# Kernel optimization log

Measured on AMD Instinct MI355X. Metric: run time of the kernel, lower is better.

The kernel has to match this reference:

```python
import jax, jax.numpy as jnp
import numpy as np

EPS = 1e-06
ALPHA = 0.1
BETA = 0.1
B, N = 2048, 4096


def setup_inputs() -> dict:
    key = jax.random.key(0)
    k1, k2, k3, k4 = jax.random.split(key, 4)
    yhat = jax.random.normal(k1, (B, N), dtype=jnp.float32)
    y = jax.random.uniform(k2, (B, N), dtype=jnp.float32)
    batch_mask = jax.random.bernoulli(k3, 0.5, (B, N))
    # neighbor matrix: entries in {0, 1, 2} remapped to {0, alpha, beta}
    raw = jax.random.randint(k4, (N, N), 0, 3)
    spots_neighbors = jnp.where(raw == 1, ALPHA, jnp.where(raw == 2, BETA, 0.0)).astype(jnp.float32)
    return {"yhat": yhat, "y": y, "batch_mask": batch_mask, "spots_neighbors": spots_neighbors}


def reference(yhat, y, batch_mask, spots_neighbors):
    # squared error everywhere: [B, N]
    sq = jnp.square(y - yhat)
    # spatial_loss[:, i] = sq @ spots_neighbors[i]  ==  sq @ spots_neighbors.T
    spatial = jnp.einsum('bn,in->bi', sq, spots_neighbors)
    # masked_error at masked positions equals sq there, so total = sq + spatial, masked
    total = sq + spatial
    m = batch_mask.astype(sq.dtype)
    cnt = jnp.sum(m)
    loss = jnp.sqrt(jnp.sum(total * m) / cnt + EPS)
    return loss
```

## Files before the change

kernel.cpp:

```cpp
#include <hip/hip_runtime.h>
#include <hip/hip_bf16.h>

typedef int   i32x4  __attribute__((ext_vector_type(4)));
typedef int   i32x8  __attribute__((ext_vector_type(8)));
typedef float f32x16 __attribute__((ext_vector_type(16)));

#define BB 2048
#define NN 4096
#define NT 32

#define SQT_OFF ((size_t)0)
#define MT_OFF  ((size_t)16*1024*1024)
#define SCAL_OFF ((size_t)32*1024*1024)
#define PART_OFF (SCAL_OFF + 1024)
#define PART2_OFF (PART_OFF + 16384)
#define NBLK_P1 (64*32)
#define NBLK_G  256

__device__ __forceinline__ unsigned f32_to_e4m3(float f) {
  if (f >= 448.0f) return 0x7eu;
  if (f < 0.015625f) return (unsigned)(int)rintf(f * 512.0f);
  unsigned u = __float_as_uint(f);
  unsigned r = u + 0x7ffffu + ((u >> 20) & 1u);
  int e = (int)((r >> 23) & 0xff) - 127;
  return ((unsigned)(e + 7) << 3) | ((r >> 20) & 7u);
}

struct P1Acc { float s1, cnt; };

template<int MODE>
__device__ __forceinline__ P1Acc p1_load_phase(
    const float* __restrict__ yhat, const float* __restrict__ y,
    const void* __restrict__ maskraw, unsigned short (*tile)[66],
    int b0, int n0, int brw, int nq)
{
  float4 yv[4], hv[4];
  float mv[4][4];
  #pragma unroll
  for (int rr = 0; rr < 4; ++rr) {
    int brow = brw + rr * 16;
    size_t idx = (size_t)(b0 + brow) * NN + n0 + nq;
    yv[rr] = *(const float4*)(y + idx);
    hv[rr] = *(const float4*)(yhat + idx);
    if (MODE == 0) {
      uchar4 t = *(const uchar4*)((const unsigned char*)maskraw + idx);
      mv[rr][0] = (float)t.x; mv[rr][1] = (float)t.y;
      mv[rr][2] = (float)t.z; mv[rr][3] = (float)t.w;
    } else if (MODE == 1) {
      int4 t = *(const int4*)((const int*)maskraw + idx);
      mv[rr][0] = (t.x != 0) ? 1.f : 0.f; mv[rr][1] = (t.y != 0) ? 1.f : 0.f;
      mv[rr][2] = (t.z != 0) ? 1.f : 0.f; mv[rr][3] = (t.w != 0) ? 1.f : 0.f;
    } else {
      float4 t = *(const float4*)((const float*)maskraw + idx);
      mv[rr][0] = (t.x != 0.f) ? 1.f : 0.f; mv[rr][1] = (t.y != 0.f) ? 1.f : 0.f;
      mv[rr][2] = (t.z != 0.f) ? 1.f : 0.f; mv[rr][3] = (t.w != 0.f) ? 1.f : 0.f;
    }
  }
  float s1 = 0.f, cnt = 0.f;
  #pragma unroll
  for (int rr = 0; rr < 4; ++rr) {
    int brow = brw + rr * 16;
    float d0 = yv[rr].x - hv[rr].x, d1 = yv[rr].y - hv[rr].y;
    float d2 = yv[rr].z - hv[rr].z, d3 = yv[rr].w - hv[rr].w;
    float sq[4] = { d0*d0, d1*d1, d2*d2, d3*d3 };
    unsigned t0 = f32_to_e4m3(sq[0]) | (mv[rr][0] != 0.f ? 0x3800u : 0u);
    unsigned t1 = f32_to_e4m3(sq[1]) | (mv[rr][1] != 0.f ? 0x3800u : 0u);
    unsigned t2 = f32_to_e4m3(sq[2]) | (mv[rr][2] != 0.f ? 0x3800u : 0u);
    unsigned t3 = f32_to_e4m3(sq[3]) | (mv[rr][3] != 0.f ? 0x3800u : 0u);
    *(uint2*)(&tile[brow][nq]) = make_uint2(t0 | (t1 << 16), t2 | (t3 << 16));
    s1 += sq[0]*mv[rr][0] + sq[1]*mv[rr][1] + sq[2]*mv[rr][2] + sq[3]*mv[rr][3];
    cnt += mv[rr][0] + mv[rr][1] + mv[rr][2] + mv[rr][3];
  }
  return { s1, cnt };
}

__global__ __launch_bounds__(256, 2) void k_pass1(
    const float* __restrict__ yhat, const float* __restrict__ y,
    const void* __restrict__ maskraw,
    unsigned char* __restrict__ SQT, unsigned char* __restrict__ MT,
    float2* __restrict__ part)
{
  __shared__ unsigned short tile[64][66];
  __shared__ float red[8];
  __shared__ unsigned mflag;
  const int tid = threadIdx.x;
  const int lane = tid & 63;
  if (tid == 0) mflag = 0;
  __syncthreads();
  {
    uint4 mb = *(const uint4*)((const unsigned char*)maskraw + tid * 16);
    unsigned f = 0;
    unsigned ws[4] = { mb.x, mb.y, mb.z, mb.w };
    #pragma unroll
    for (int q = 0; q < 4; ++q) {
      unsigned w = ws[q];
      bool h3f = ((w & 0xffu) == 0x3fu) | (((w >> 8) & 0xffu) == 0x3fu) |
                 (((w >> 16) & 0xffu) == 0x3fu) | ((w >> 24) == 0x3fu);
      f |= h3f ? 1u : 0u;
      f |= ((w & 0xffffff00u) != 0u) ? 2u : 0u;
    }
    bool a1 = __any((int)(f & 1)), a2 = __any((int)(f & 2));
    if (lane == 0) {
      unsigned g = (a1 ? 1u : 0u) | (a2 ? 2u : 0u);
      if (g) atomicOr(&mflag, g);
    }
  }
  __syncthreads();
  const unsigned mf = mflag;
  const int mode = (mf & 1) ? 2 : ((mf & 2) ? 0 : 1);

  const int n0 = blockIdx.x * 64;
  const int b0 = blockIdx.y * 64;
  const int nq = (tid & 15) * 4;
  const int brw = tid >> 4;
  P1Acc a;
  if (mode == 0)      a = p1_load_phase<0>(yhat, y, maskraw, tile, b0, n0, brw, nq);
  else if (mode == 1) a = p1_load_phase<1>(yhat, y, maskraw, tile, b0, n0, brw, nq);
  else                a = p1_load_phase<2>(yhat, y, maskraw, tile, b0, n0, brw, nq);
  __syncthreads();
  {
    int nrow = tid >> 2;
    int cb   = tid & 3;
    int grow = n0 + nrow;
    unsigned us[4], um[4];
    #pragma unroll
    for (int q = 0; q < 4; ++q) {
      unsigned v0 = tile[cb*16 + q*4 + 0][nrow];
      unsigned v1 = tile[cb*16 + q*4 + 1][nrow];
      unsigned v2 = tile[cb*16 + q*4 + 2][nrow];
      unsigned v3 = tile[cb*16 + q*4 + 3][nrow];
      us[q] = (v0 & 0xffu) | ((v1 & 0xffu) << 8) | ((v2 & 0xffu) << 16) | ((v3 & 0xffu) << 24);
      um[q] = (v0 >> 8) | ((v1 >> 8) << 8) | ((v2 >> 8) << 16) | ((v3 >> 8) << 24);
    }
    size_t off = (size_t)(grow >> 7) * 262144 + (size_t)(b0 >> 6) * 8192
               + (size_t)cb * 2048 + (size_t)(grow & 127) * 16;
    *(uint4*)(SQT + off) = make_uint4(us[0], us[1], us[2], us[3]);
    *(uint4*)(MT  + off) = make_uint4(um[0], um[1], um[2], um[3]);
  }
  float s1 = a.s1, cnt = a.cnt;
  #pragma unroll
  for (int off = 32; off >= 1; off >>= 1) {
    s1  += __shfl_down(s1,  off, 64);
    cnt += __shfl_down(cnt, off, 64);
  }
  int wv = tid >> 6;
  if ((tid & 63) == 0) { red[wv] = s1; red[4 + wv] = cnt; }
  __syncthreads();
  if (tid == 0)
    part[blockIdx.y * gridDim.x + blockIdx.x] =
        make_float2(red[0] + red[1] + red[2] + red[3],
                    red[4] + red[5] + red[6] + red[7]);
}

__global__ __launch_bounds__(512, 2) void k_gemm(
    const unsigned char* __restrict__ MT,
    const unsigned char* __restrict__ SQT,
    const float* __restrict__ W,
    float* __restrict__ part2)
{
  extern __shared__ char lds[];
  const int tid = threadIdx.x;
  const int lane = tid & 63;
  const int wave = tid >> 6;
  const int wm  = wave >> 2;
  const int wmB = wm * 128;
  const int wnB = (wave & 3) * 64;
  const int l31 = lane & 31;
  const int lch2 = (lane >> 5) * 2;

  const int bid = blockIdx.x;
  const int swz = (bid & 7) * 32 + (bid >> 3);
  const int nb = swz & 15, ib = swz >> 4;
  const int n0 = nb * 256, i0 = ib * 256;

  const unsigned char* aSrc = MT  + (size_t)ib * 524288;
  const unsigned char* bSrc = SQT + (size_t)nb * 524288;
  const int tid16 = tid * 16;

#define STG(c, s) \
  _Pragma("unroll") for (int j = 0; j < 2; ++j) { \
    __builtin_amdgcn_global_load_lds( \
      (const __attribute__((address_space(1))) unsigned int*)( \
          aSrc + (size_t)j * 262144 + (size_t)(s) * 8192 + tid16), \
      (__attribute__((address_space(3))) unsigned int*)(lds + (c) * 16384 + j * 8192 + tid16), \
      16, 0, 0); \
    __builtin_amdgcn_global_load_lds( \
      (const __attribute__((address_space(1))) unsigned int*)( \
          bSrc + (size_t)j * 262144 + (size_t)(s) * 8192 + tid16), \
      (__attribute__((address_space(3))) unsigned int*)(lds + 65536 + (c) * 16384 + j * 8192 + tid16), \
      16, 0, 0); }

#define WPF(k) { \
    float4 wtmp = *((const float4*)(W + (size_t)(i0 + (k)*8 + (tid >> 6)) * NN + n0) + (tid & 63)); \
    asm volatile("" :: "v"(wtmp.x), "v"(wtmp.y), "v"(wtmp.z), "v"(wtmp.w)); }

#define RDA2(d0, d1, bufA, mgb) { \
    const char* p0 = (bufA) + wm*8192 + lch2*2048 + ((mgb)*32 + l31)*16; \
    const char* p1 = p0 + 512; \
    i32x4 lo0 = *(const i32x4*)p0; i32x4 hi0 = *(const i32x4*)(p0 + 2048); \
    i32x4 lo1 = *(const i32x4*)p1; i32x4 hi1 = *(const i32x4*)(p1 + 2048); \
    d0 = __builtin_shufflevector(lo0, hi0, 0, 1, 2, 3, 4, 5, 6, 7); \
    d1 = __builtin_shufflevector(lo1, hi1, 0, 1, 2, 3, 4, 5, 6, 7); }
#define RDB(d, bufB, ng) { \
    int rg = wnB + (ng)*32; \
    const char* p = (bufB) + (rg >> 7)*8192 + lch2*2048 + ((rg & 127) + l31)*16; \
    i32x4 lo = *(const i32x4*)p; i32x4 hi = *(const i32x4*)(p + 2048); \
    d = __builtin_shufflevector(lo, hi, 0, 1, 2, 3, 4, 5, 6, 7); }

#define MM(mg, ng, A, B) \
  acc[mg][ng] = __builtin_amdgcn_mfma_scale_f32_32x32x64_f8f6f4( \
      A, B, acc[mg][ng], 0, 0, 0, 0x7f7f7f7f, 0, 0x7f7f7f7f)

#define TILE_BODY(c) { \
    const char* bufA = lds + (c) * 16384; \
    const char* bufB = lds + 65536 + (c) * 16384; \
    i32x8 a0, a1, a2, a3, b0, b1; \
    RDA2(a0, a1, bufA, 0); RDB(b0, bufB, 0); \
    RDA2(a2, a3, bufA, 2); RDB(b1, bufB, 1); \
    MM(0, 0, a0, b0); MM(1, 0, a1, b0); MM(2, 0, a2, b0); MM(3, 0, a3, b0); \
    MM(0, 1, a0, b1); MM(1, 1, a1, b1); MM(2, 1, a2, b1); MM(3, 1, a3, b1); }

  f32x16 acc[4][2] = {};

  STG(0, 0); WPF(0);
  STG(1, 1); WPF(1);
  STG(2, 2); WPF(2);

  #pragma unroll 1
  for (int t = 0; t < NT - 2; ++t) {
    asm volatile("s_waitcnt vmcnt(11)" ::: "memory");
    __builtin_amdgcn_s_barrier();
    __builtin_amdgcn_sched_barrier(0);
    if (t < NT - 3) { STG((t + 3) & 3, t + 3); WPF(t + 3); }
    TILE_BODY(t & 3);
  }
  asm volatile("s_waitcnt vmcnt(6)" ::: "memory");
  __builtin_amdgcn_s_barrier();
  __builtin_amdgcn_sched_barrier(0);
  TILE_BODY(2);
  asm volatile("s_waitcnt vmcnt(1)" ::: "memory");
  __builtin_amdgcn_s_barrier();
  __builtin_amdgcn_sched_barrier(0);
  TILE_BODY(3);
#undef STG
#undef WPF
#undef RDA2
#undef RDB
#undef MM
#undef TILE_BODY

  float local = 0.0f;
  #pragma unroll
  for (int mg = 0; mg < 4; ++mg) {
    int rbase = i0 + wmB + mg * 32 + (lane >> 5) * 4;
    #pragma unroll
    for (int ng = 0; ng < 2; ++ng) {
      int nn = n0 + wnB + ng * 32 + l31;
      const float* wp = W + (size_t)rbase * NN + nn;
      #pragma unroll
      for (int reg = 0; reg < 16; ++reg) {
        int roff = (reg & 3) + 8 * (reg >> 2);
        local += acc[mg][ng][reg] * wp[(size_t)roff * NN];
      }
    }
  }
  #pragma unroll
  for (int off = 32; off >= 1; off >>= 1)
    local += __shfl_down(local, off, 64);
  float* wpart = (float*)lds;
  __syncthreads();
  if (lane == 0) wpart[wave] = local;
  __syncthreads();
  if (tid == 0) {
    float s = 0.f;
    #pragma unroll
    for (int i = 0; i < 8; ++i) s += wpart[i];
    part2[bid] = s;
  }
}

__global__ __launch_bounds__(256) void k_finalize(
    const float2* __restrict__ part, const float* __restrict__ part2,
    float* __restrict__ out)
{
  __shared__ float rs[4], rc[4];
  float s1 = 0.f, cnt = 0.f;
  for (int i = threadIdx.x; i < NBLK_P1; i += 256) {
    float2 p = part[i];
    s1 += p.x; cnt += p.y;
  }
  for (int i = threadIdx.x; i < NBLK_G; i += 256)
    s1 += part2[i];
  #pragma unroll
  for (int off = 32; off >= 1; off >>= 1) {
    s1  += __shfl_down(s1,  off, 64);
    cnt += __shfl_down(cnt, off, 64);
  }
  int wv = threadIdx.x >> 6;
  if ((threadIdx.x & 63) == 0) { rs[wv] = s1; rc[wv] = cnt; }
  __syncthreads();
  if (threadIdx.x == 0) {
    float S = rs[0] + rs[1] + rs[2] + rs[3];
    float C = rc[0] + rc[1] + rc[2] + rc[3];
    out[0] = sqrtf(S / C + 1e-6f);
  }
}

__global__ void k_sentinel(float* out) { out[0] = 1.2345e8f; }

extern "C" void kernel_launch(void* const* d_in, const int* in_sizes, int n_in,
                              void* d_out, int out_size, void* d_ws, size_t ws_size,
                              hipStream_t stream) {
  const float* yhat = (const float*)d_in[0];
  const float* y    = (const float*)d_in[1];
  const void*  mask = d_in[2];
  const float* W    = (const float*)d_in[3];
  float* out = (float*)d_out;

  const size_t need = PART2_OFF + (size_t)NBLK_G * 4;
  if (ws_size < need) { k_sentinel<<<1, 1, 0, stream>>>(out); return; }

  char* ws = (char*)d_ws;
  unsigned char* SQT = (unsigned char*)(ws + SQT_OFF);
  unsigned char* MTp = (unsigned char*)(ws + MT_OFF);
  float2* part = (float2*)(ws + PART_OFF);
  float* part2 = (float*)(ws + PART2_OFF);

  (void)hipFuncSetAttribute((const void*)k_gemm,
                            hipFuncAttributeMaxDynamicSharedMemorySize, 131072);

  k_pass1<<<dim3(NN/64, BB/64), 256, 0, stream>>>(yhat, y, mask, SQT, MTp, part);
  k_gemm<<<NBLK_G, 512, 131072, stream>>>(MTp, SQT, W, part2);
  k_finalize<<<1, 256, 0, stream>>>(part, part2, out);
}
```

Before: 72.60 us.

## Load A fragments directly to registers, double-buffer only B in LDS

The GEMM kernel now reads the A operand (mask tile) straight from global memory into per-wave registers instead of staging it through LDS, and keeps only B in a two-stage LDS double buffer, cutting shared memory from 128KB to 32KB. The W prefetch into cache is dropped, the pipeline depth goes from four stages to two with full vmcnt(0) waits each step, and MFMA blocks are wrapped in s_setprio. This reduces LDS traffic and footprint but exposes more global-load latency because the prefetch distance is shorter.

```diff
diff --git a/kernel.cpp b/kernel.cpp
--- a/kernel.cpp
+++ b/kernel.cpp
@@ -173,81 +173,73 @@
   const int nb = swz & 15, ib = swz >> 4;
   const int n0 = nb * 256, i0 = ib * 256;
 
-  const unsigned char* aSrc = MT  + (size_t)ib * 524288;
   const unsigned char* bSrc = SQT + (size_t)nb * 524288;
+  const unsigned char* aLane = MT + (size_t)ib * 524288 + (size_t)wm * 262144
+                             + (size_t)lch2 * 2048 + (size_t)l31 * 16;
   const int tid16 = tid * 16;
 
-#define STG(c, s) \
+#define STG_B(c, s) \
   _Pragma("unroll") for (int j = 0; j < 2; ++j) { \
     __builtin_amdgcn_global_load_lds( \
       (const __attribute__((address_space(1))) unsigned int*)( \
-          aSrc + (size_t)j * 262144 + (size_t)(s) * 8192 + tid16), \
+          bSrc + (size_t)j * 262144 + (size_t)(s) * 8192 + tid16), \
       (__attribute__((address_space(3))) unsigned int*)(lds + (c) * 16384 + j * 8192 + tid16), \
-      16, 0, 0); \
-    __builtin_amdgcn_global_load_lds( \
-      (const __attribute__((address_space(1))) unsigned int*)( \
-          bSrc + (size_t)j * 262144 + (size_t)(s) * 8192 + tid16), \
-      (__attribute__((address_space(3))) unsigned int*)(lds + 65536 + (c) * 16384 + j * 8192 + tid16), \
       16, 0, 0); }
 
-#define WPF(k) { \
-    float4 wtmp = *((const float4*)(W + (size_t)(i0 + (k)*8 + (tid >> 6)) * NN + n0) + (tid & 63)); \
-    asm volatile("" :: "v"(wtmp.x), "v"(wtmp.y), "v"(wtmp.z), "v"(wtmp.w)); }
-
-#define RDA2(d0, d1, bufA, mgb) { \
-    const char* p0 = (bufA) + wm*8192 + lch2*2048 + ((mgb)*32 + l31)*16; \
-    const char* p1 = p0 + 512; \
+#define ALD(dst, s) \
+  _Pragma("unroll") for (int mg = 0; mg < 4; ++mg) { \
+    const unsigned char* p = aLane + (size_t)(s) * 8192 + mg * 512; \
+    i32x4 lo = *(const i32x4*)p; \
+    i32x4 hi = *(const i32x4*)(p + 2048); \
+    dst[mg] = __builtin_shufflevector(lo, hi, 0, 1, 2, 3, 4, 5, 6, 7); }
+
+#define RDB(d0r, d1r, c) { \
+    int rg0 = wnB; \
+    const char* p0 = lds + (c)*16384 + (rg0 >> 7)*8192 + lch2*2048 + ((rg0 & 127) + l31)*16; \
     i32x4 lo0 = *(const i32x4*)p0; i32x4 hi0 = *(const i32x4*)(p0 + 2048); \
+    d0r = __builtin_shufflevector(lo0, hi0, 0, 1, 2, 3, 4, 5, 6, 7); \
+    int rg1 = wnB + 32; \
+    const char* p1 = lds + (c)*16384 + (rg1 >> 7)*8192 + lch2*2048 + ((rg1 & 127) + l31)*16; \
     i32x4 lo1 = *(const i32x4*)p1; i32x4 hi1 = *(const i32x4*)(p1 + 2048); \
-    d0 = __builtin_shufflevector(lo0, hi0, 0, 1, 2, 3, 4, 5, 6, 7); \
-    d1 = __builtin_shufflevector(lo1, hi1, 0, 1, 2, 3, 4, 5, 6, 7); }
-#define RDB(d, bufB, ng) { \
-    int rg = wnB + (ng)*32; \
-    const char* p = (bufB) + (rg >> 7)*8192 + lch2*2048 + ((rg & 127) + l31)*16; \
-    i32x4 lo = *(const i32x4*)p; i32x4 hi = *(const i32x4*)(p + 2048); \
-    d = __builtin_shufflevector(lo, hi, 0, 1, 2, 3, 4, 5, 6, 7); }
-
-#define MM(mg, ng, A, B) \
-  acc[mg][ng] = __builtin_amdgcn_mfma_scale_f32_32x32x64_f8f6f4( \
-      A, B, acc[mg][ng], 0, 0, 0, 0x7f7f7f7f, 0, 0x7f7f7f7f)
-
-#define TILE_BODY(c) { \
-    const char* bufA = lds + (c) * 16384; \
-    const char* bufB = lds + 65536 + (c) * 16384; \
-    i32x8 a0, a1, a2, a3, b0, b1; \
-    RDA2(a0, a1, bufA, 0); RDB(b0, bufB, 0); \
-    RDA2(a2, a3, bufA, 2); RDB(b1, bufB, 1); \
-    MM(0, 0, a0, b0); MM(1, 0, a1, b0); MM(2, 0, a2, b0); MM(3, 0, a3, b0); \
-    MM(0, 1, a0, b1); MM(1, 1, a1, b1); MM(2, 1, a2, b1); MM(3, 1, a3, b1); }
-
+    d1r = __builtin_shufflevector(lo1, hi1, 0, 1, 2, 3, 4, 5, 6, 7); }
+
+#define MFMA8(AF, B0, B1) \
+  __builtin_amdgcn_s_setprio(1); \
+  _Pragma("unroll") for (int mg = 0; mg < 4; ++mg) { \
+    acc[mg][0] = __builtin_amdgcn_mfma_scale_f32_32x32x64_f8f6f4( \
+        AF[mg], B0, acc[mg][0], 0, 0, 0, 0x7f7f7f7f, 0, 0x7f7f7f7f); \
+    acc[mg][1] = __builtin_amdgcn_mfma_scale_f32_32x32x64_f8f6f4( \
+        AF[mg], B1, acc[mg][1], 0, 0, 0, 0x7f7f7f7f, 0, 0x7f7f7f7f); } \
+  __builtin_amdgcn_s_setprio(0)
+
+#define TOPSYNC \
+  asm volatile("s_waitcnt vmcnt(0)" ::: "memory"); \
+  __builtin_amdgcn_s_barrier(); \
+  __builtin_amdgcn_sched_barrier(0)
+
+  i32x8 aX[4], aY[4], b0r, b1r;
   f32x16 acc[4][2] = {};
 
-  STG(0, 0); WPF(0);
-  STG(1, 1); WPF(1);
-  STG(2, 2); WPF(2);
+  ALD(aX, 0);
+  STG_B(0, 0);
 
   #pragma unroll 1
-  for (int t = 0; t < NT - 2; ++t) {
-    asm volatile("s_waitcnt vmcnt(11)" ::: "memory");
-    __builtin_amdgcn_s_barrier();
-    __builtin_amdgcn_sched_barrier(0);
-    if (t < NT - 3) { STG((t + 3) & 3, t + 3); WPF(t + 3); }
-    TILE_BODY(t & 3);
-  }
-  asm volatile("s_waitcnt vmcnt(6)" ::: "memory");
-  __builtin_amdgcn_s_barrier();
-  __builtin_amdgcn_sched_barrier(0);
-  TILE_BODY(2);
-  asm volatile("s_waitcnt vmcnt(1)" ::: "memory");
-  __builtin_amdgcn_s_barrier();
-  __builtin_amdgcn_sched_barrier(0);
-  TILE_BODY(3);
-#undef STG
-#undef WPF
-#undef RDA2
+  for (int tp = 0; tp < NT; tp += 2) {
+    TOPSYNC;
+    ALD(aY, tp + 1);
+    STG_B(1, tp + 1);
+    RDB(b0r, b1r, 0);
+    MFMA8(aX, b0r, b1r);
+    TOPSYNC;
+    if (tp + 2 < NT) { ALD(aX, tp + 2); STG_B(0, tp + 2); }
+    RDB(b0r, b1r, 1);
+    MFMA8(aY, b0r, b1r);
+  }
+#undef STG_B
+#undef ALD
 #undef RDB
-#undef MM
-#undef TILE_BODY
+#undef MFMA8
+#undef TOPSYNC
 
   float local = 0.0f;
   #pragma unroll
@@ -327,9 +319,9 @@
   float* part2 = (float*)(ws + PART2_OFF);
 
   (void)hipFuncSetAttribute((const void*)k_gemm,
-                            hipFuncAttributeMaxDynamicSharedMemorySize, 131072);
+                            hipFuncAttributeMaxDynamicSharedMemorySize, 32768);
 
   k_pass1<<<dim3(NN/64, BB/64), 256, 0, stream>>>(yhat, y, mask, SQT, MTp, part);
-  k_gemm<<<NBLK_G, 512, 131072, stream>>>(MTp, SQT, W, part2);
+  k_gemm<<<NBLK_G, 512, 32768, stream>>>(MTp, SQT, W, part2);
   k_finalize<<<1, 256, 0, stream>>>(part, part2, out);
 }
```

Result: slower. 75.82 us (+4.4%).

## Use 1024-thread GEMM blocks with 2x2 MFMA tiles per wave and 3-stage buffering

Applied to the files above, without the earlier changes.

Doubles the GEMM block to 16 waves so each wave owns a 64x64 output tile (4 accumulators) instead of 128x64 (8). The LDS pipeline drops from 4 stages to 3, and the W prefetch into cache is removed. MFMA sections are wrapped in s_setprio. The aim is more waves to hide latency and lower register pressure, at the cost of each wave doing more LDS reads per MFMA and having shallower prefetch.

```diff
diff --git a/kernel.cpp b/kernel.cpp
--- a/kernel.cpp
+++ b/kernel.cpp
@@ -152,7 +152,7 @@
                     red[4] + red[5] + red[6] + red[7]);
 }
 
-__global__ __launch_bounds__(512, 2) void k_gemm(
+__global__ __launch_bounds__(1024) void k_gemm(
     const unsigned char* __restrict__ MT,
     const unsigned char* __restrict__ SQT,
     const float* __restrict__ W,
@@ -163,8 +163,7 @@
   const int lane = tid & 63;
   const int wave = tid >> 6;
   const int wm  = wave >> 2;
-  const int wmB = wm * 128;
-  const int wnB = (wave & 3) * 64;
+  const int wn  = wave & 3;
   const int l31 = lane & 31;
   const int lch2 = (lane >> 5) * 2;
 
@@ -176,92 +175,72 @@
   const unsigned char* aSrc = MT  + (size_t)ib * 524288;
   const unsigned char* bSrc = SQT + (size_t)nb * 524288;
   const int tid16 = tid * 16;
-
-#define STG(c, s) \
-  _Pragma("unroll") for (int j = 0; j < 2; ++j) { \
-    __builtin_amdgcn_global_load_lds( \
-      (const __attribute__((address_space(1))) unsigned int*)( \
-          aSrc + (size_t)j * 262144 + (size_t)(s) * 8192 + tid16), \
-      (__attribute__((address_space(3))) unsigned int*)(lds + (c) * 16384 + j * 8192 + tid16), \
-      16, 0, 0); \
-    __builtin_amdgcn_global_load_lds( \
-      (const __attribute__((address_space(1))) unsigned int*)( \
-          bSrc + (size_t)j * 262144 + (size_t)(s) * 8192 + tid16), \
-      (__attribute__((address_space(3))) unsigned int*)(lds + 65536 + (c) * 16384 + j * 8192 + tid16), \
-      16, 0, 0); }
-
-#define WPF(k) { \
-    float4 wtmp = *((const float4*)(W + (size_t)(i0 + (k)*8 + (tid >> 6)) * NN + n0) + (tid & 63)); \
-    asm volatile("" :: "v"(wtmp.x), "v"(wtmp.y), "v"(wtmp.z), "v"(wtmp.w)); }
-
-#define RDA2(d0, d1, bufA, mgb) { \
-    const char* p0 = (bufA) + wm*8192 + lch2*2048 + ((mgb)*32 + l31)*16; \
-    const char* p1 = p0 + 512; \
-    i32x4 lo0 = *(const i32x4*)p0; i32x4 hi0 = *(const i32x4*)(p0 + 2048); \
-    i32x4 lo1 = *(const i32x4*)p1; i32x4 hi1 = *(const i32x4*)(p1 + 2048); \
-    d0 = __builtin_shufflevector(lo0, hi0, 0, 1, 2, 3, 4, 5, 6, 7); \
-    d1 = __builtin_shufflevector(lo1, hi1, 0, 1, 2, 3, 4, 5, 6, 7); }
-#define RDB(d, bufB, ng) { \
-    int rg = wnB + (ng)*32; \
-    const char* p = (bufB) + (rg >> 7)*8192 + lch2*2048 + ((rg & 127) + l31)*16; \
+  const int jrb = tid16 >> 13;
+  const int joff = tid16 & 8191;
+
+#define STG_A(c, s) \
+  __builtin_amdgcn_global_load_lds( \
+    (const __attribute__((address_space(1))) unsigned int*)( \
+        aSrc + (size_t)jrb * 262144 + (size_t)(s) * 8192 + joff), \
+    (__attribute__((address_space(3))) unsigned int*)(lds + (c) * 16384 + tid16), 16, 0, 0)
+#define STG_B(c, s) \
+  __builtin_amdgcn_global_load_lds( \
+    (const __attribute__((address_space(1))) unsigned int*)( \
+        bSrc + (size_t)jrb * 262144 + (size_t)(s) * 8192 + joff), \
+    (__attribute__((address_space(3))) unsigned int*)(lds + 49152 + (c) * 16384 + tid16), 16, 0, 0)
+
+#define RD(dst, base, row) { \
+    const char* p = (base) + ((row) >> 7) * 8192 + lch2 * 2048 + (((row) & 127) + l31) * 16; \
     i32x4 lo = *(const i32x4*)p; i32x4 hi = *(const i32x4*)(p + 2048); \
-    d = __builtin_shufflevector(lo, hi, 0, 1, 2, 3, 4, 5, 6, 7); }
-
-#define MM(mg, ng, A, B) \
-  acc[mg][ng] = __builtin_amdgcn_mfma_scale_f32_32x32x64_f8f6f4( \
-      A, B, acc[mg][ng], 0, 0, 0, 0x7f7f7f7f, 0, 0x7f7f7f7f)
-
-#define TILE_BODY(c) { \
-    const char* bufA = lds + (c) * 16384; \
-    const char* bufB = lds + 65536 + (c) * 16384; \
-    i32x8 a0, a1, a2, a3, b0, b1; \
-    RDA2(a0, a1, bufA, 0); RDB(b0, bufB, 0); \
-    RDA2(a2, a3, bufA, 2); RDB(b1, bufB, 1); \
-    MM(0, 0, a0, b0); MM(1, 0, a1, b0); MM(2, 0, a2, b0); MM(3, 0, a3, b0); \
-    MM(0, 1, a0, b1); MM(1, 1, a1, b1); MM(2, 1, a2, b1); MM(3, 1, a3, b1); }
-
-  f32x16 acc[4][2] = {};
-
-  STG(0, 0); WPF(0);
-  STG(1, 1); WPF(1);
-  STG(2, 2); WPF(2);
+    dst = __builtin_shufflevector(lo, hi, 0, 1, 2, 3, 4, 5, 6, 7); }
+
+#define MM(accv, A, B) \
+  accv = __builtin_amdgcn_mfma_scale_f32_32x32x64_f8f6f4( \
+      A, B, accv, 0, 0, 0, 0x7f7f7f7f, 0, 0x7f7f7f7f)
+
+  i32x8 a0, a1, b0, b1;
+  f32x16 acc00 = {}, acc01 = {}, acc10 = {}, acc11 = {};
+
+  const int rA0 = wm * 64,      rA1 = wm * 64 + 32;
+  const int rB0 = wn * 64,      rB1 = wn * 64 + 32;
+
+  STG_A(0, 0); STG_B(0, 0);
+  STG_A(1, 1); STG_B(1, 1);
 
   #pragma unroll 1
-  for (int t = 0; t < NT - 2; ++t) {
-    asm volatile("s_waitcnt vmcnt(11)" ::: "memory");
+  for (int t = 0; t < NT; ++t) {
+    const int cur = t % 3;
+    const int dst = (t + 2) % 3;
+    if (t < NT - 1) { asm volatile("s_waitcnt vmcnt(2)" ::: "memory"); }
+    else            { asm volatile("s_waitcnt vmcnt(0)" ::: "memory"); }
     __builtin_amdgcn_s_barrier();
     __builtin_amdgcn_sched_barrier(0);
-    if (t < NT - 3) { STG((t + 3) & 3, t + 3); WPF(t + 3); }
-    TILE_BODY(t & 3);
-  }
-  asm volatile("s_waitcnt vmcnt(6)" ::: "memory");
-  __builtin_amdgcn_s_barrier();
-  __builtin_amdgcn_sched_barrier(0);
-  TILE_BODY(2);
-  asm volatile("s_waitcnt vmcnt(1)" ::: "memory");
-  __builtin_amdgcn_s_barrier();
-  __builtin_amdgcn_sched_barrier(0);
-  TILE_BODY(3);
-#undef STG
-#undef WPF
-#undef RDA2
-#undef RDB
+    if (t < NT - 2) { STG_A(dst, t + 2); STG_B(dst, t + 2); }
+    const char* bufA = lds + cur * 16384;
+    const char* bufB = lds + 49152 + cur * 16384;
+    RD(a0, bufA, rA0); RD(a1, bufA, rA1);
+    RD(b0, bufB, rB0); RD(b1, bufB, rB1);
+    __builtin_amdgcn_s_setprio(1);
+    MM(acc00, a0, b0); MM(acc01, a0, b1);
+    MM(acc10, a1, b0); MM(acc11, a1, b1);
+    __builtin_amdgcn_s_setprio(0);
+  }
+#undef STG_A
+#undef STG_B
+#undef RD
 #undef MM
-#undef TILE_BODY
 
   float local = 0.0f;
-  #pragma unroll
-  for (int mg = 0; mg < 4; ++mg) {
-    int rbase = i0 + wmB + mg * 32 + (lane >> 5) * 4;
+  {
+    const int rb0 = i0 + wm * 64 + (lane >> 5) * 4;
+    const int cb0 = n0 + wn * 64 + l31;
     #pragma unroll
-    for (int ng = 0; ng < 2; ++ng) {
-      int nn = n0 + wnB + ng * 32 + l31;
-      const float* wp = W + (size_t)rbase * NN + nn;
-      #pragma unroll
-      for (int reg = 0; reg < 16; ++reg) {
-        int roff = (reg & 3) + 8 * (reg >> 2);
-        local += acc[mg][ng][reg] * wp[(size_t)roff * NN];
-      }
+    for (int reg = 0; reg < 16; ++reg) {
+      int roff = (reg & 3) + 8 * (reg >> 2);
+      const float* w0 = W + (size_t)(rb0 + roff) * NN + cb0;
+      const float* w1 = W + (size_t)(rb0 + 32 + roff) * NN + cb0;
+      local += acc00[reg] * w0[0] + acc01[reg] * w0[32]
+             + acc10[reg] * w1[0] + acc11[reg] * w1[32];
     }
   }
   #pragma unroll
@@ -274,7 +253,7 @@
   if (tid == 0) {
     float s = 0.f;
     #pragma unroll
-    for (int i = 0; i < 8; ++i) s += wpart[i];
+    for (int i = 0; i < 16; ++i) s += wpart[i];
     part2[bid] = s;
   }
 }
@@ -327,9 +306,9 @@
   float* part2 = (float*)(ws + PART2_OFF);
 
   (void)hipFuncSetAttribute((const void*)k_gemm,
-                            hipFuncAttributeMaxDynamicSharedMemorySize, 131072);
+                            hipFuncAttributeMaxDynamicSharedMemorySize, 98304);
 
   k_pass1<<<dim3(NN/64, BB/64), 256, 0, stream>>>(yhat, y, mask, SQT, MTp, part);
-  k_gemm<<<NBLK_G, 512, 131072, stream>>>(MTp, SQT, W, part2);
+  k_gemm<<<NBLK_G, 1024, 98304, stream>>>(MTp, SQT, W, part2);
   k_finalize<<<1, 256, 0, stream>>>(part, part2, out);
 }
```

Result: faster. 66.62 us (-8.2%).
